# Kernel tuning notes

Measured on AMD Instinct MI355X. Metric: run time of the kernel, lower is better.

Reference implementation:

```python
import jax, jax.numpy as jnp
import numpy as np

CONTEXT_LENGTHS = [1, 3, 5, 7]
PADS = [(f - 1) // 2 for f in CONTEXT_LENGTHS]  # p(f) for odd f
B, H, L, DK = 2, 8, 1024, 64
C = H * DK  # conv channels = d_k * n_heads


def _conv1d(x, w, b, pad):
    # x: (b, C, L), w: (C, C, f), b: (C,) -- torch Conv1d semantics
    y = jax.lax.conv_general_dilated(
        x, w, window_strides=(1,), padding=[(pad, pad)],
        dimension_numbers=("NCH", "OIH", "NCH"))
    return y + b[None, :, None]


def _plane(a, w, b, pad, out_len):
    # Faithful to: conv(a.reshape(b, h*d_k, -1)).reshape(b, h, -1, d_k)[:, :, :out_len, :]
    bsz, h, l, d = a.shape
    y = _conv1d(a.reshape(bsz, h * d, l), w, b, pad)
    return y.reshape(bsz, h, -1, d)[:, :, :out_len, :]


def setup_inputs() -> dict:
    key = jax.random.key(0)
    ks = jax.random.split(key, 12)
    inp = {
        "Q": jax.random.normal(ks[0], (B, H, L, DK), jnp.float32),
        "K": jax.random.normal(ks[1], (B, H, L, DK), jnp.float32),
        "V": jax.random.normal(ks[2], (B, H, L, DK), jnp.float32),
        # causal mask: True = masked
        "attn_mask": jnp.broadcast_to(
            jnp.triu(jnp.ones((L, L), jnp.bool_), k=1), (B, H, L, L)),
    }
    for i, f in enumerate(CONTEXT_LENGTHS):
        scale = 1.0 / np.sqrt(C * f)
        inp[f"conv_w{i}"] = jax.random.normal(ks[3 + i], (C, C, f), jnp.float32) * scale
        inp[f"conv_b{i}"] = jax.random.normal(ks[7 + i], (C,), jnp.float32) * scale
    return inp


def reference(Q, K, V, attn_mask,
              conv_w0, conv_b0, conv_w1, conv_b1,
              conv_w2, conv_b2, conv_w3, conv_b3):
    ws = [conv_w0, conv_w1, conv_w2, conv_w3]
    bs = [conv_b0, conv_b1, conv_b2, conv_b3]
    b, h, l, d_k = Q.shape
    l_k = K.shape[2]
    p = len(CONTEXT_LENGTHS)
    Q_l = [_plane(Q, ws[i], bs[i], PADS[i], l) for i in range(p)]
    K_l = [_plane(K, ws[i], bs[i], PADS[i], l_k) for i in range(p)]
    # replicate torch.cat(dim=0).reshape(b, h, p, l, d) exactly (row-major)
    Q_p = jnp.concatenate(Q_l, axis=0).reshape(b, h, p, l, d_k)
    K_p = jnp.concatenate(K_l, axis=0).reshape(b, h, p, l_k, d_k)
    scores = jnp.einsum("bhpqd,bhpkd->bhpqk", Q_p, K_p) / np.sqrt(d_k).astype(np.float32)
    scores = jnp.where(attn_mask[:, :, None, :, :], jnp.float32(-1e9), scores)
    attn = jax.nn.softmax(scores, axis=-1)
    attn = jnp.max(attn, axis=2)  # max over planes -> (b,h,q,k)
    context = jnp.einsum("bhqk,bhkd->bhqd", attn, V)
    return (context, attn)
```

## Files before the change

### kernel.cpp

```cpp
#include <hip/hip_runtime.h>
#include <math.h>

#define C_CH 512
#define L_SEQ 1024
#define DK 64
#define NP 4
#define SC2 0.1803368801111f

typedef __attribute__((ext_vector_type(8))) short short8;
typedef __attribute__((ext_vector_type(4))) float f32x4;

__device__ __forceinline__ unsigned short f2bf(float f) {
    union { float f; unsigned u; } v; v.f = f;
    unsigned u = v.u;
    u += 0x7FFFu + ((u >> 16) & 1u);
    return (unsigned short)(u >> 16);
}

__device__ __forceinline__ void unpack_tri(int t, int& qt, int& kt) {
    int q = (int)((sqrtf(8.f * t + 1.f) - 1.f) * 0.5f);
    while ((q + 1) * (q + 2) / 2 <= t) q++;
    while (q * (q + 1) / 2 > t) q--;
    qt = q;
    kt = t - q * (q + 1) / 2;
}

__global__ __launch_bounds__(256)
void prep_w_kernel(const float* __restrict__ w0, const float* __restrict__ w1,
                   const float* __restrict__ w2, const float* __restrict__ w3,
                   unsigned short* __restrict__ Wb) {
    int tg = blockIdx.y;
    int plane, t;
    if (tg < 1)      { plane = 0; t = tg; }
    else if (tg < 4) { plane = 1; t = tg - 1; }
    else if (tg < 9) { plane = 2; t = tg - 4; }
    else             { plane = 3; t = tg - 9; }
    const float* W = (plane == 0) ? w0 : (plane == 1) ? w1 : (plane == 2) ? w2 : w3;
    const int f = (plane == 0) ? 1 : (plane == 1) ? 3 : (plane == 2) ? 5 : 7;

    int co = blockIdx.x * 32 + (threadIdx.x >> 3);
    int c8 = threadIdx.x & 7;
    for (int it = 0; it < 8; it++) {
        int ci = c8 * 8 + it * 64;
        unsigned short o[8];
#pragma unroll
        for (int j = 0; j < 8; j++)
            o[j] = f2bf(W[(size_t)(co * C_CH + ci + j) * f + t]);
        *(short8*)&Wb[((size_t)tg * C_CH + co) * C_CH + ci] = *(short8*)o;
    }
}

__global__ __launch_bounds__(256)
void prep_x_kernel(const float* __restrict__ Qin, const float* __restrict__ Kin,
                   unsigned short* __restrict__ Xt) {
    int tb = blockIdx.z;
    int tensor = tb >> 1, b = tb & 1;
    const float* X = (tensor ? Kin : Qin) + (size_t)b * C_CH * L_SEQ;
    unsigned short* O = Xt + (size_t)tb * 1032 * C_CH;

    int pos0 = blockIdx.x * 64;
    int ci0  = blockIdx.y * 64;
    int tid = threadIdx.x;

    __shared__ float tile[64][65];
    int tx = tid & 15, ty = tid >> 4;
#pragma unroll
    for (int rr = 0; rr < 4; rr++) {
        int ci_l = ty + rr * 16;
        float4 v = *(const float4*)&X[(size_t)(ci0 + ci_l) * L_SEQ + pos0 + tx * 4];
        tile[tx * 4 + 0][ci_l] = v.x;
        tile[tx * 4 + 1][ci_l] = v.y;
        tile[tx * 4 + 2][ci_l] = v.z;
        tile[tx * 4 + 3][ci_l] = v.w;
    }
    __syncthreads();
#pragma unroll
    for (int pp = 0; pp < 2; pp++) {
        int pos_l = (tid >> 3) + pp * 32;
        int cg = (tid & 7) * 8;
        unsigned short o[8];
#pragma unroll
        for (int j = 0; j < 8; j++) o[j] = f2bf(tile[pos_l][cg + j]);
        *(short8*)&O[(size_t)(pos0 + pos_l + 4) * C_CH + ci0 + cg] = *(short8*)o;
    }
    if (blockIdx.x == 0) {
        int r = tid >> 6, cc = tid & 63;
        O[(size_t)r * C_CH + ci0 + cc] = 0;
    }
    if (blockIdx.x == 15) {
        int r = tid >> 6, cc = tid & 63;
        O[(size_t)(1028 + r) * C_CH + ci0 + cc] = 0;
    }
}

__global__ __launch_bounds__(256)
void conv_mfma_kernel(const unsigned short* __restrict__ Xt,
                      const unsigned short* __restrict__ Wb,
                      const float* __restrict__ b0, const float* __restrict__ b1,
                      const float* __restrict__ b2, const float* __restrict__ b3,
                      unsigned short* __restrict__ Qp, unsigned short* __restrict__ Kp) {
    const int fs[4]   = {1, 3, 5, 7};
    const int toff[4] = {0, 1, 4, 9};
    int id = blockIdx.x;
    int plane, rel;
    if (id < 128)      { plane = 0; rel = id; }
    else if (id < 256) { plane = 1; rel = id - 128; }
    else if (id < 384) { plane = 3; rel = id - 256; }
    else               { plane = 2; rel = id - 384; }
    int co0  = (rel & 3) * 128;
    int pos0 = ((rel >> 2) & 7) * 128;
    int tb   = rel >> 5;
    int tensor = tb >> 1, b = tb & 1;
    const int f   = fs[plane];
    const int pad = (f - 1) >> 1;
    const int n   = f * 16;
    const float* bias = (plane == 0) ? b0 : (plane == 1) ? b1 : (plane == 2) ? b2 : b3;
    unsigned short* Out = tensor ? Kp : Qp;
    const unsigned short* Xbase = Xt + (size_t)tb * 1032 * C_CH;

    __shared__ __align__(16) unsigned short As[2][4096];
    __shared__ __align__(16) unsigned short Bs[2][4096];

    int tid  = threadIdx.x;
    int w    = tid >> 6;
    int lane = tid & 63;
    int l15  = lane & 15;
    int quad = lane >> 4;
    int wm = (w & 1) * 64;
    int wn = (w >> 1) * 64;
    int rowL = tid >> 2;
    int cS   = tid & 3;

    int woff[2];
#pragma unroll
    for (int rep = 0; rep < 2; rep++) {
        int r = rowL + rep * 64;
        int line = r >> 1;
        int sl = (((r & 1) << 2) | cS) ^ (line & 7);
        woff[rep] = line * 64 + sl * 8;
    }
    int aoff[4], boff[4];
#pragma unroll
    for (int mi = 0; mi < 4; mi++) {
        int r = wm + mi * 16 + l15;
        int line = r >> 1;
        aoff[mi] = line * 64 + ((((r & 1) << 2) | quad) ^ (line & 7)) * 8;
        int r2 = wn + mi * 16 + l15;
        int line2 = r2 >> 1;
        boff[mi] = line2 * 64 + ((((r2 & 1) << 2) | quad) ^ (line2 & 7)) * 8;
    }

    f32x4 acc[4][4];
#pragma unroll
    for (int mi = 0; mi < 4; mi++)
#pragma unroll
        for (int ni = 0; ni < 4; ni++) acc[mi][ni] = (f32x4){0.f, 0.f, 0.f, 0.f};

    short8 pA[2], pB[2];
    {
        const unsigned short* Wsl = Wb + ((size_t)toff[plane] * C_CH + co0) * C_CH;
        const unsigned short* Xsl = Xbase + (size_t)(pos0 - pad + 4) * C_CH;
#pragma unroll
        for (int rep = 0; rep < 2; rep++) {
            int r = rowL + rep * 64;
            pA[rep] = *(const short8*)&Wsl[(size_t)r * C_CH + cS * 8];
            pB[rep] = *(const short8*)&Xsl[(size_t)r * C_CH + cS * 8];
        }
    }

    for (int it = 0; it < n; it++) {
        int cur = it & 1;
        *(short8*)&As[cur][woff[0]] = pA[0];
        *(short8*)&As[cur][woff[1]] = pA[1];
        *(short8*)&Bs[cur][woff[0]] = pB[0];
        *(short8*)&Bs[cur][woff[1]] = pB[1];
        __syncthreads();

        if (it + 1 < n) {
            int t = (it + 1) >> 4, cc = (it + 1) & 15;
            const unsigned short* Wsl =
                Wb + ((size_t)(toff[plane] + t) * C_CH + co0) * C_CH + cc * 32;
            const unsigned short* Xsl =
                Xbase + (size_t)(pos0 + t - pad + 4) * C_CH + cc * 32;
#pragma unroll
            for (int rep = 0; rep < 2; rep++) {
                int r = rowL + rep * 64;
                pA[rep] = *(const short8*)&Wsl[(size_t)r * C_CH + cS * 8];
                pB[rep] = *(const short8*)&Xsl[(size_t)r * C_CH + cS * 8];
            }
        }

        short8 af[4], bf[4];
#pragma unroll
        for (int mi = 0; mi < 4; mi++) af[mi] = *(const short8*)&As[cur][aoff[mi]];
#pragma unroll
        for (int ni = 0; ni < 4; ni++) bf[ni] = *(const short8*)&Bs[cur][boff[ni]];
#pragma unroll
        for (int mi = 0; mi < 4; mi++)
#pragma unroll
            for (int ni = 0; ni < 4; ni++)
                acc[mi][ni] = __builtin_amdgcn_mfma_f32_16x16x32_bf16(
                    af[mi], bf[ni], acc[mi][ni], 0, 0, 0);
    }

#pragma unroll
    for (int mi = 0; mi < 4; mi++)
#pragma unroll
        for (int r = 0; r < 4; r++) {
            int co = co0 + wm + mi * 16 + quad * 4 + r;
            int h = co >> 6, cl = co & 63;
            float bv = bias[co];
            size_t sbase = (size_t)((b * 8 + h) * NP + plane) * L_SEQ * DK;
#pragma unroll
            for (int ni = 0; ni < 4; ni++) {
                int pos = pos0 + wn + ni * 16 + l15;
                int l = cl * 16 + (pos >> 6);
                int d = pos & 63;
                Out[sbase + (size_t)l * DK + d] = f2bf(acc[mi][ni][r] + bv);
            }
        }
}

__global__ __launch_bounds__(256)
void attn_stats_kernel(const unsigned short* __restrict__ Qb,
                       const unsigned short* __restrict__ Kb,
                       float* __restrict__ lsum) {
    int qt, kt;
    unpack_tri(blockIdx.x, qt, kt);
    int bh = blockIdx.y;
    int tid = threadIdx.x;
    int q0 = qt * 64, k0 = kt * 64;
    bool diag = (kt == qt);

    int b2 = bh >> 3, h2 = bh & 7;
    int plane  = b2 * 2 + (h2 >> 2);
    int b_orig = (h2 >> 1) & 1;
    int h_base = (h2 & 1) * 4;
    int w = tid >> 6, lane = tid & 63, l15 = lane & 15, quad = lane >> 4;

    float l[NP][4];
#pragma unroll
    for (int p = 0; p < NP; p++)
        for (int r = 0; r < 4; r++) l[p][r] = 0.f;

#pragma unroll
    for (int p = 0; p < NP; p++) {
        size_t slice = (size_t)((b_orig * 8 + h_base + p) * NP + plane);
        const unsigned short* kb = Kb + slice * L_SEQ * DK;
        const unsigned short* qrow =
            Qb + (slice * L_SEQ + (size_t)(q0 + w * 16 + l15)) * DK + quad * 8;
        short8 qa0 = *(const short8*)(qrow);
        short8 qa1 = *(const short8*)(qrow + 32);

        f32x4 c[4];
#pragma unroll
        for (int s = 0; s < 4; s++) {
            const unsigned short* kr = kb + (size_t)(k0 + s * 16 + l15) * DK + quad * 8;
            short8 kb0 = *(const short8*)(kr);
            short8 kb1 = *(const short8*)(kr + 32);
            f32x4 acc = {0.f, 0.f, 0.f, 0.f};
            acc = __builtin_amdgcn_mfma_f32_16x16x32_bf16(qa0, kb0, acc, 0, 0, 0);
            acc = __builtin_amdgcn_mfma_f32_16x16x32_bf16(qa1, kb1, acc, 0, 0, 0);
            c[s] = acc;
        }
#pragma unroll
        for (int r = 0; r < 4; r++) {
            int row_local = quad * 4 + r + w * 16;
#pragma unroll
            for (int s = 0; s < 4; s++) {
                float x = c[s][r] * SC2;
                if (diag && (s * 16 + l15 > row_local)) x = -1e30f;
                l[p][r] += exp2f(x);
            }
        }
    }

    size_t base = (size_t)(bh * 16 + qt) * (NP * 64);
#pragma unroll
    for (int p = 0; p < NP; p++)
#pragma unroll
        for (int r = 0; r < 4; r++) {
            float ll = l[p][r];
            ll += __shfl_xor(ll, 1);
            ll += __shfl_xor(ll, 2);
            ll += __shfl_xor(ll, 4);
            ll += __shfl_xor(ll, 8);
            if (l15 == 0)
                unsafeAtomicAdd(&lsum[base + p * 64 + (w * 16 + quad * 4 + r)], ll);
        }
}

__global__ __launch_bounds__(256)
void attn_combine_kernel(const float* __restrict__ lsum,
                         float* __restrict__ fstats,
                         float* __restrict__ out_ctx, float* __restrict__ out_attn) {
    int qt = blockIdx.x, bh = blockIdx.y;
    int tid = threadIdx.x;
    size_t sb = (size_t)(bh * 16 + qt) * (NP * 64);
    fstats[sb + tid] = __log2f(lsum[sb + tid]);

    int r = tid >> 2, c = (tid & 3) * 16;
    float4 z = make_float4(0.f, 0.f, 0.f, 0.f);
    size_t cbase = ((size_t)bh * L_SEQ + qt * 64 + r) * DK + c;
#pragma unroll
    for (int j = 0; j < 4; j++)
        *(float4*)&out_ctx[cbase + j * 4] = z;

    int kz = (qt + 1) * 64;
    size_t abase = ((size_t)bh * L_SEQ + qt * 64 + r) * L_SEQ;
    for (int k = kz + (tid & 3) * 4; k < L_SEQ; k += 16)
        *(float4*)&out_attn[abase + k] = z;
}

__global__ __launch_bounds__(256)
void attn_apply_kernel(const unsigned short* __restrict__ Qb,
                       const unsigned short* __restrict__ Kb,
                       const float* __restrict__ V,
                       const float* __restrict__ fstats,
                       float* __restrict__ out_ctx, float* __restrict__ out_attn) {
    int qt, kt;
    unpack_tri(blockIdx.x, qt, kt);
    int bh = blockIdx.y;
    int tid = threadIdx.x;
    int q0 = qt * 64, k0 = kt * 64;
    bool diag = (kt == qt);

    int b2 = bh >> 3, h2 = bh & 7;
    int plane  = b2 * 2 + (h2 >> 2);
    int b_orig = (h2 >> 1) & 1;
    int h_base = (h2 & 1) * 4;
    int w = tid >> 6, lane = tid & 63, l15 = lane & 15, quad = lane >> 4;

    __shared__ float zsm[NP * 64];
    __shared__ __align__(16) unsigned short ast[64 * 80];
    __shared__ __align__(16) unsigned short vts[64 * 80];

    zsm[tid] = fstats[(size_t)(bh * 16 + qt) * (NP * 64) + tid];

    const unsigned short* kbase[NP];
    short8 qa[NP][2];
#pragma unroll
    for (int p = 0; p < NP; p++) {
        size_t slice = (size_t)((b_orig * 8 + h_base + p) * NP + plane);
        kbase[p] = Kb + slice * L_SEQ * DK;
        const unsigned short* qrow =
            Qb + (slice * L_SEQ + (size_t)(q0 + w * 16 + l15)) * DK + quad * 8;
        qa[p][0] = *(const short8*)(qrow);
        qa[p][1] = *(const short8*)(qrow + 32);
    }

    {
        int kl = tid >> 2, db = (tid & 3) * 16;
        const float* vr = V + ((size_t)bh * L_SEQ + k0 + kl) * DK + db;
        float vv[16];
        *(float4*)&vv[0]  = *(const float4*)(vr);
        *(float4*)&vv[4]  = *(const float4*)(vr + 4);
        *(float4*)&vv[8]  = *(const float4*)(vr + 8);
        *(float4*)&vv[12] = *(const float4*)(vr + 12);
#pragma unroll
        for (int j = 0; j < 16; j++)
            vts[(db + j) * 80 + kl] = f2bf(vv[j]);
    }
    __syncthreads();

    float run[4][4];
#pragma unroll
    for (int s = 0; s < 4; s++)
        for (int r = 0; r < 4; r++) run[s][r] = -1e30f;

#pragma unroll
    for (int p = 0; p < NP; p++) {
        f32x4 c[4];
#pragma unroll
        for (int s = 0; s < 4; s++) {
            const unsigned short* kr =
                kbase[p] + (size_t)(k0 + s * 16 + l15) * DK + quad * 8;
            short8 kb0 = *(const short8*)(kr);
            short8 kb1 = *(const short8*)(kr + 32);
            f32x4 acc = {0.f, 0.f, 0.f, 0.f};
            acc = __builtin_amdgcn_mfma_f32_16x16x32_bf16(qa[p][0], kb0, acc, 0, 0, 0);
            acc = __builtin_amdgcn_mfma_f32_16x16x32_bf16(qa[p][1], kb1, acc, 0, 0, 0);
            c[s] = acc;
        }
#pragma unroll
        for (int r = 0; r < 4; r++) {
            float zp = zsm[p * 64 + (quad * 4 + r + w * 16)];
#pragma unroll
            for (int s = 0; s < 4; s++)
                run[s][r] = fmaxf(run[s][r], c[s][r] * SC2 - zp);
        }
    }

#pragma unroll
    for (int s = 0; s < 4; s++)
#pragma unroll
        for (int r = 0; r < 4; r++) {
            int qloc = w * 16 + quad * 4 + r;
            bool masked = diag && (s * 16 + l15 > qloc);
            float a = masked ? 0.f : exp2f(run[s][r]);
            out_attn[((size_t)bh * L_SEQ + q0 + qloc) * L_SEQ + k0 + s * 16 + l15] = a;
            ast[qloc * 80 + s * 16 + l15] = f2bf(a);
        }

    f32x4 ctxc[4];
#pragma unroll
    for (int ds = 0; ds < 4; ds++) ctxc[ds] = (f32x4){0.f, 0.f, 0.f, 0.f};
    short8 af0 = *(const short8*)&ast[(w * 16 + l15) * 80 + quad * 8];
    short8 af1 = *(const short8*)&ast[(w * 16 + l15) * 80 + 32 + quad * 8];
#pragma unroll
    for (int ds = 0; ds < 4; ds++) {
        short8 bf0 = *(const short8*)&vts[(ds * 16 + l15) * 80 + quad * 8];
        short8 bf1 = *(const short8*)&vts[(ds * 16 + l15) * 80 + 32 + quad * 8];
        ctxc[ds] = __builtin_amdgcn_mfma_f32_16x16x32_bf16(af0, bf0, ctxc[ds], 0, 0, 0);
        ctxc[ds] = __builtin_amdgcn_mfma_f32_16x16x32_bf16(af1, bf1, ctxc[ds], 0, 0, 0);
    }

#pragma unroll
    for (int ds = 0; ds < 4; ds++)
#pragma unroll
        for (int r = 0; r < 4; r++) {
            int qg = q0 + w * 16 + quad * 4 + r;
            unsafeAtomicAdd(&out_ctx[((size_t)bh * L_SEQ + qg) * DK + ds * 16 + l15],
                            ctxc[ds][r]);
        }
}

extern "C" void kernel_launch(void* const* d_in, const int* in_sizes, int n_in,
                              void* d_out, int out_size, void* d_ws, size_t ws_size,
                              hipStream_t stream) {
    const float* Q  = (const float*)d_in[0];
    const float* K  = (const float*)d_in[1];
    const float* V  = (const float*)d_in[2];
    const float* w0 = (const float*)d_in[4];
    const float* b0 = (const float*)d_in[5];
    const float* w1 = (const float*)d_in[6];
    const float* b1 = (const float*)d_in[7];
    const float* w2 = (const float*)d_in[8];
    const float* b2 = (const float*)d_in[9];
    const float* w3 = (const float*)d_in[10];
    const float* b3 = (const float*)d_in[11];

    char* ws = (char*)d_ws;
    unsigned short* Wb = (unsigned short*)(ws);
    unsigned short* Xt = (unsigned short*)(ws + 8388608);
    unsigned short* Qp = (unsigned short*)(ws + 12615680);
    unsigned short* Kp = (unsigned short*)(ws + 21004288);
    float* lsum   = (float*)(ws + 8388608);
    float* fstats = (float*)(ws + 8388608 + 262144);

    float* out_ctx  = (float*)d_out;
    float* out_attn = out_ctx + 1048576;

    prep_w_kernel<<<dim3(16, 16), 256, 0, stream>>>(w0, w1, w2, w3, Wb);
    prep_x_kernel<<<dim3(16, 8, 4), 256, 0, stream>>>(Q, K, Xt);
    conv_mfma_kernel<<<dim3(512), 256, 0, stream>>>(Xt, Wb, b0, b1, b2, b3, Qp, Kp);
    hipMemsetAsync(lsum, 0, 262144, stream);
    attn_stats_kernel<<<dim3(136, 16), 256, 0, stream>>>(Qp, Kp, lsum);
    attn_combine_kernel<<<dim3(16, 16), 256, 0, stream>>>(lsum, fstats, out_ctx, out_attn);
    attn_apply_kernel<<<dim3(136, 16), 256, 0, stream>>>(Qp, Kp, V, fstats,
                                                         out_ctx, out_attn);
}
```

Measured before the change: 355.0 us.

## Group key tiles per block and replace atomics with partial-sum reduction

The stats and apply kernels now give each block a contiguous run of up to four key tiles for one query tile, instead of one (q,k) tile pair per block. This cuts the grid from 136 to 40 blocks per head and reuses the loaded Q fragments across tiles. Atomic adds for the row sums and context are replaced by per-group partial buffers, which the combine kernel and a new ctx_reduce kernel sum, so the memset goes away. The trade-off is fewer blocks, which lowers parallelism, plus an extra launch and more workspace traffic. The apply loop uses double-buffered V smem with a single barrier per iteration.

```diff
diff --git a/kernel.cpp b/kernel.cpp
--- a/kernel.cpp
+++ b/kernel.cpp
@@ -17,12 +17,20 @@
     return (unsigned short)(u >> 16);
 }
 
-__device__ __forceinline__ void unpack_tri(int t, int& qt, int& kt) {
-    int q = (int)((sqrtf(8.f * t + 1.f) - 1.f) * 0.5f);
-    while ((q + 1) * (q + 2) / 2 <= t) q++;
-    while (q * (q + 1) / 2 > t) q--;
+__device__ __forceinline__ void unpack_group(int G, int& qt, int& kt0, int& kt1,
+                                             int& j, int& ng) {
+    int q = 15, cum = 0, jj = 0;
+    for (; q >= 0; q--) {
+        int g = (q + 4) >> 2;
+        if (G < cum + g) { jj = G - cum; break; }
+        cum += g;
+    }
     qt = q;
-    kt = t - q * (q + 1) / 2;
+    ng = (q + 4) >> 2;
+    j = jj;
+    int n = q + 1;
+    kt0 = (jj * n) / ng;
+    kt1 = ((jj + 1) * n) / ng;
 }
 
 __global__ __launch_bounds__(256)
@@ -44,8 +52,8 @@
         int ci = c8 * 8 + it * 64;
         unsigned short o[8];
 #pragma unroll
-        for (int j = 0; j < 8; j++)
-            o[j] = f2bf(W[(size_t)(co * C_CH + ci + j) * f + t]);
+        for (int jj = 0; jj < 8; jj++)
+            o[jj] = f2bf(W[(size_t)(co * C_CH + ci + jj) * f + t]);
         *(short8*)&Wb[((size_t)tg * C_CH + co) * C_CH + ci] = *(short8*)o;
     }
 }
@@ -80,7 +88,7 @@
         int cg = (tid & 7) * 8;
         unsigned short o[8];
 #pragma unroll
-        for (int j = 0; j < 8; j++) o[j] = f2bf(tile[pos_l][cg + j]);
+        for (int jj = 0; jj < 8; jj++) o[jj] = f2bf(tile[pos_l][cg + jj]);
         *(short8*)&O[(size_t)(pos0 + pos_l + 4) * C_CH + ci0 + cg] = *(short8*)o;
     }
     if (blockIdx.x == 0) {
@@ -224,13 +232,12 @@
 __global__ __launch_bounds__(256)
 void attn_stats_kernel(const unsigned short* __restrict__ Qb,
                        const unsigned short* __restrict__ Kb,
-                       float* __restrict__ lsum) {
-    int qt, kt;
-    unpack_tri(blockIdx.x, qt, kt);
+                       float* __restrict__ pl) {
+    int qt, kt0, kt1, j, ng;
+    unpack_group(blockIdx.x, qt, kt0, kt1, j, ng);
     int bh = blockIdx.y;
     int tid = threadIdx.x;
-    int q0 = qt * 64, k0 = kt * 64;
-    bool diag = (kt == qt);
+    int q0 = qt * 64;
 
     int b2 = bh >> 3, h2 = bh & 7;
     int plane  = b2 * 2 + (h2 >> 2);
@@ -238,44 +245,54 @@
     int h_base = (h2 & 1) * 4;
     int w = tid >> 6, lane = tid & 63, l15 = lane & 15, quad = lane >> 4;
 
+    const unsigned short* kbase[NP];
+    short8 qa[NP][2];
+#pragma unroll
+    for (int p = 0; p < NP; p++) {
+        size_t slice = (size_t)((b_orig * 8 + h_base + p) * NP + plane);
+        kbase[p] = Kb + slice * L_SEQ * DK;
+        const unsigned short* qrow =
+            Qb + (slice * L_SEQ + (size_t)(q0 + w * 16 + l15)) * DK + quad * 8;
+        qa[p][0] = *(const short8*)(qrow);
+        qa[p][1] = *(const short8*)(qrow + 32);
+    }
+
     float l[NP][4];
 #pragma unroll
     for (int p = 0; p < NP; p++)
         for (int r = 0; r < 4; r++) l[p][r] = 0.f;
 
-#pragma unroll
-    for (int p = 0; p < NP; p++) {
-        size_t slice = (size_t)((b_orig * 8 + h_base + p) * NP + plane);
-        const unsigned short* kb = Kb + slice * L_SEQ * DK;
-        const unsigned short* qrow =
-            Qb + (slice * L_SEQ + (size_t)(q0 + w * 16 + l15)) * DK + quad * 8;
-        short8 qa0 = *(const short8*)(qrow);
-        short8 qa1 = *(const short8*)(qrow + 32);
-
-        f32x4 c[4];
-#pragma unroll
-        for (int s = 0; s < 4; s++) {
-            const unsigned short* kr = kb + (size_t)(k0 + s * 16 + l15) * DK + quad * 8;
-            short8 kb0 = *(const short8*)(kr);
-            short8 kb1 = *(const short8*)(kr + 32);
-            f32x4 acc = {0.f, 0.f, 0.f, 0.f};
-            acc = __builtin_amdgcn_mfma_f32_16x16x32_bf16(qa0, kb0, acc, 0, 0, 0);
-            acc = __builtin_amdgcn_mfma_f32_16x16x32_bf16(qa1, kb1, acc, 0, 0, 0);
-            c[s] = acc;
-        }
-#pragma unroll
-        for (int r = 0; r < 4; r++) {
-            int row_local = quad * 4 + r + w * 16;
+    for (int kt = kt0; kt < kt1; kt++) {
+        int k0 = kt * 64;
+        bool diag = (kt == qt);
+#pragma unroll
+        for (int p = 0; p < NP; p++) {
+            f32x4 c[4];
 #pragma unroll
             for (int s = 0; s < 4; s++) {
-                float x = c[s][r] * SC2;
-                if (diag && (s * 16 + l15 > row_local)) x = -1e30f;
-                l[p][r] += exp2f(x);
-            }
-        }
-    }
-
-    size_t base = (size_t)(bh * 16 + qt) * (NP * 64);
+                const unsigned short* kr =
+                    kbase[p] + (size_t)(k0 + s * 16 + l15) * DK + quad * 8;
+                short8 kb0 = *(const short8*)(kr);
+                short8 kb1 = *(const short8*)(kr + 32);
+                f32x4 acc = {0.f, 0.f, 0.f, 0.f};
+                acc = __builtin_amdgcn_mfma_f32_16x16x32_bf16(qa[p][0], kb0, acc, 0, 0, 0);
+                acc = __builtin_amdgcn_mfma_f32_16x16x32_bf16(qa[p][1], kb1, acc, 0, 0, 0);
+                c[s] = acc;
+            }
+#pragma unroll
+            for (int r = 0; r < 4; r++) {
+                int row_local = quad * 4 + r + w * 16;
+#pragma unroll
+                for (int s = 0; s < 4; s++) {
+                    float x = c[s][r] * SC2;
+                    if (diag && (s * 16 + l15 > row_local)) x = -1e30f;
+                    l[p][r] += exp2f(x);
+                }
+            }
+        }
+    }
+
+    size_t base = ((size_t)(bh * 16 + qt) * 4 + j) * 256;
 #pragma unroll
     for (int p = 0; p < NP; p++)
 #pragma unroll
@@ -286,26 +303,26 @@
             ll += __shfl_xor(ll, 4);
             ll += __shfl_xor(ll, 8);
             if (l15 == 0)
-                unsafeAtomicAdd(&lsum[base + p * 64 + (w * 16 + quad * 4 + r)], ll);
-        }
-}
-
-__global__ __launch_bounds__(256)
-void attn_combine_kernel(const float* __restrict__ lsum,
+                pl[base + p * 64 + (w * 16 + quad * 4 + r)] = ll;
+        }
+}
+
+__global__ __launch_bounds__(256)
+void attn_combine_kernel(const float* __restrict__ pl,
                          float* __restrict__ fstats,
-                         float* __restrict__ out_ctx, float* __restrict__ out_attn) {
+                         float* __restrict__ out_attn) {
     int qt = blockIdx.x, bh = blockIdx.y;
     int tid = threadIdx.x;
-    size_t sb = (size_t)(bh * 16 + qt) * (NP * 64);
-    fstats[sb + tid] = __log2f(lsum[sb + tid]);
-
-    int r = tid >> 2, c = (tid & 3) * 16;
+    int ng = (qt + 4) >> 2;
+    size_t sb = (size_t)(bh * 16 + qt) * 4 * 256;
+
+    float l = 0.f;
+    for (int g = 0; g < ng; g++)
+        l += pl[sb + (size_t)g * 256 + tid];
+    fstats[(size_t)(bh * 16 + qt) * 256 + tid] = __log2f(l);
+
+    int r = tid >> 2;
     float4 z = make_float4(0.f, 0.f, 0.f, 0.f);
-    size_t cbase = ((size_t)bh * L_SEQ + qt * 64 + r) * DK + c;
-#pragma unroll
-    for (int j = 0; j < 4; j++)
-        *(float4*)&out_ctx[cbase + j * 4] = z;
-
     int kz = (qt + 1) * 64;
     size_t abase = ((size_t)bh * L_SEQ + qt * 64 + r) * L_SEQ;
     for (int k = kz + (tid & 3) * 4; k < L_SEQ; k += 16)
@@ -317,13 +334,12 @@
                        const unsigned short* __restrict__ Kb,
                        const float* __restrict__ V,
                        const float* __restrict__ fstats,
-                       float* __restrict__ out_ctx, float* __restrict__ out_attn) {
-    int qt, kt;
-    unpack_tri(blockIdx.x, qt, kt);
+                       float* __restrict__ pctx, float* __restrict__ out_attn) {
+    int qt, kt0, kt1, j, ng;
+    unpack_group(blockIdx.x, qt, kt0, kt1, j, ng);
     int bh = blockIdx.y;
     int tid = threadIdx.x;
-    int q0 = qt * 64, k0 = kt * 64;
-    bool diag = (kt == qt);
+    int q0 = qt * 64;
 
     int b2 = bh >> 3, h2 = bh & 7;
     int plane  = b2 * 2 + (h2 >> 2);
@@ -333,9 +349,9 @@
 
     __shared__ float zsm[NP * 64];
     __shared__ __align__(16) unsigned short ast[64 * 80];
-    __shared__ __align__(16) unsigned short vts[64 * 80];
-
-    zsm[tid] = fstats[(size_t)(bh * 16 + qt) * (NP * 64) + tid];
+    __shared__ __align__(16) unsigned short vts[2][64 * 80];
+
+    zsm[tid] = fstats[(size_t)(bh * 16 + qt) * 256 + tid];
 
     const unsigned short* kbase[NP];
     short8 qa[NP][2];
@@ -349,80 +365,118 @@
         qa[p][1] = *(const short8*)(qrow + 32);
     }
 
-    {
-        int kl = tid >> 2, db = (tid & 3) * 16;
-        const float* vr = V + ((size_t)bh * L_SEQ + k0 + kl) * DK + db;
-        float vv[16];
-        *(float4*)&vv[0]  = *(const float4*)(vr);
-        *(float4*)&vv[4]  = *(const float4*)(vr + 4);
-        *(float4*)&vv[8]  = *(const float4*)(vr + 8);
-        *(float4*)&vv[12] = *(const float4*)(vr + 12);
-#pragma unroll
-        for (int j = 0; j < 16; j++)
-            vts[(db + j) * 80 + kl] = f2bf(vv[j]);
-    }
-    __syncthreads();
-
-    float run[4][4];
-#pragma unroll
-    for (int s = 0; s < 4; s++)
-        for (int r = 0; r < 4; r++) run[s][r] = -1e30f;
-
-#pragma unroll
-    for (int p = 0; p < NP; p++) {
-        f32x4 c[4];
-#pragma unroll
-        for (int s = 0; s < 4; s++) {
-            const unsigned short* kr =
-                kbase[p] + (size_t)(k0 + s * 16 + l15) * DK + quad * 8;
-            short8 kb0 = *(const short8*)(kr);
-            short8 kb1 = *(const short8*)(kr + 32);
-            f32x4 acc = {0.f, 0.f, 0.f, 0.f};
-            acc = __builtin_amdgcn_mfma_f32_16x16x32_bf16(qa[p][0], kb0, acc, 0, 0, 0);
-            acc = __builtin_amdgcn_mfma_f32_16x16x32_bf16(qa[p][1], kb1, acc, 0, 0, 0);
-            c[s] = acc;
-        }
-#pragma unroll
-        for (int r = 0; r < 4; r++) {
-            float zp = zsm[p * 64 + (quad * 4 + r + w * 16)];
-#pragma unroll
-            for (int s = 0; s < 4; s++)
-                run[s][r] = fmaxf(run[s][r], c[s][r] * SC2 - zp);
-        }
-    }
-
-#pragma unroll
-    for (int s = 0; s < 4; s++)
+    f32x4 ctxc[4];
+#pragma unroll
+    for (int ds = 0; ds < 4; ds++) ctxc[ds] = (f32x4){0.f, 0.f, 0.f, 0.f};
+
+    for (int kt = kt0; kt < kt1; kt++) {
+        int k0 = kt * 64;
+        bool diag = (kt == qt);
+        unsigned short* vb = vts[kt & 1];
+
+        {
+            int kl = tid >> 2, db = (tid & 3) * 16;
+            const float* vr = V + ((size_t)bh * L_SEQ + k0 + kl) * DK + db;
+            float vv[16];
+            *(float4*)&vv[0]  = *(const float4*)(vr);
+            *(float4*)&vv[4]  = *(const float4*)(vr + 4);
+            *(float4*)&vv[8]  = *(const float4*)(vr + 8);
+            *(float4*)&vv[12] = *(const float4*)(vr + 12);
+#pragma unroll
+            for (int jj = 0; jj < 16; jj++)
+                vb[(db + jj) * 80 + kl] = f2bf(vv[jj]);
+        }
+        __syncthreads();
+
+        float run[4][4];
+#pragma unroll
+        for (int s = 0; s < 4; s++)
+            for (int r = 0; r < 4; r++) run[s][r] = -1e30f;
+
+#pragma unroll
+        for (int p = 0; p < NP; p++) {
+            f32x4 c[4];
+#pragma unroll
+            for (int s = 0; s < 4; s++) {
+                const unsigned short* kr =
+                    kbase[p] + (size_t)(k0 + s * 16 + l15) * DK + quad * 8;
+                short8 kb0 = *(const short8*)(kr);
+                short8 kb1 = *(const short8*)(kr + 32);
+                f32x4 acc = {0.f, 0.f, 0.f, 0.f};
+                acc = __builtin_amdgcn_mfma_f32_16x16x32_bf16(qa[p][0], kb0, acc, 0, 0, 0);
+                acc = __builtin_amdgcn_mfma_f32_16x16x32_bf16(qa[p][1], kb1, acc, 0, 0, 0);
+                c[s] = acc;
+            }
+#pragma unroll
+            for (int r = 0; r < 4; r++) {
+                float zp = zsm[p * 64 + (quad * 4 + r + w * 16)];
+#pragma unroll
+                for (int s = 0; s < 4; s++)
+                    run[s][r] = fmaxf(run[s][r], c[s][r] * SC2 - zp);
+            }
+        }
+
+#pragma unroll
+        for (int s = 0; s < 4; s++)
+#pragma unroll
+            for (int r = 0; r < 4; r++) {
+                int qloc = w * 16 + quad * 4 + r;
+                bool masked = diag && (s * 16 + l15 > qloc);
+                float a = masked ? 0.f : exp2f(run[s][r]);
+                out_attn[((size_t)bh * L_SEQ + q0 + qloc) * L_SEQ + k0 + s * 16 + l15] = a;
+                ast[qloc * 80 + s * 16 + l15] = f2bf(a);
+            }
+
+        short8 af0 = *(const short8*)&ast[(w * 16 + l15) * 80 + quad * 8];
+        short8 af1 = *(const short8*)&ast[(w * 16 + l15) * 80 + 32 + quad * 8];
+#pragma unroll
+        for (int ds = 0; ds < 4; ds++) {
+            short8 bf0 = *(const short8*)&vb[(ds * 16 + l15) * 80 + quad * 8];
+            short8 bf1 = *(const short8*)&vb[(ds * 16 + l15) * 80 + 32 + quad * 8];
+            ctxc[ds] = __builtin_amdgcn_mfma_f32_16x16x32_bf16(af0, bf0, ctxc[ds], 0, 0, 0);
+            ctxc[ds] = __builtin_amdgcn_mfma_f32_16x16x32_bf16(af1, bf1, ctxc[ds], 0, 0, 0);
+        }
+    }
+
+    size_t pbase = ((size_t)(bh * 16 + qt) * 4 + j) * 4096;
+#pragma unroll
+    for (int ds = 0; ds < 4; ds++)
 #pragma unroll
         for (int r = 0; r < 4; r++) {
             int qloc = w * 16 + quad * 4 + r;
-            bool masked = diag && (s * 16 + l15 > qloc);
-            float a = masked ? 0.f : exp2f(run[s][r]);
-            out_attn[((size_t)bh * L_SEQ + q0 + qloc) * L_SEQ + k0 + s * 16 + l15] = a;
-            ast[qloc * 80 + s * 16 + l15] = f2bf(a);
-        }
-
-    f32x4 ctxc[4];
-#pragma unroll
-    for (int ds = 0; ds < 4; ds++) ctxc[ds] = (f32x4){0.f, 0.f, 0.f, 0.f};
-    short8 af0 = *(const short8*)&ast[(w * 16 + l15) * 80 + quad * 8];
-    short8 af1 = *(const short8*)&ast[(w * 16 + l15) * 80 + 32 + quad * 8];
-#pragma unroll
-    for (int ds = 0; ds < 4; ds++) {
-        short8 bf0 = *(const short8*)&vts[(ds * 16 + l15) * 80 + quad * 8];
-        short8 bf1 = *(const short8*)&vts[(ds * 16 + l15) * 80 + 32 + quad * 8];
-        ctxc[ds] = __builtin_amdgcn_mfma_f32_16x16x32_bf16(af0, bf0, ctxc[ds], 0, 0, 0);
-        ctxc[ds] = __builtin_amdgcn_mfma_f32_16x16x32_bf16(af1, bf1, ctxc[ds], 0, 0, 0);
-    }
-
-#pragma unroll
-    for (int ds = 0; ds < 4; ds++)
-#pragma unroll
-        for (int r = 0; r < 4; r++) {
-            int qg = q0 + w * 16 + quad * 4 + r;
-            unsafeAtomicAdd(&out_ctx[((size_t)bh * L_SEQ + qg) * DK + ds * 16 + l15],
-                            ctxc[ds][r]);
-        }
+            pctx[pbase + (size_t)qloc * 64 + ds * 16 + l15] = ctxc[ds][r];
+        }
+}
+
+__global__ __launch_bounds__(256)
+void ctx_reduce_kernel(const float* __restrict__ pctx, float* __restrict__ out_ctx) {
+    int qt = blockIdx.x, bh = blockIdx.y;
+    int tid = threadIdx.x;
+    int ng = (qt + 4) >> 2;
+    size_t base = (size_t)(bh * 16 + qt) * 4 * 4096;
+    int row = tid >> 2, c = (tid & 3) * 16;
+    size_t off = (size_t)row * 64 + c;
+
+    float4 a0 = *(const float4*)&pctx[base + off];
+    float4 a1 = *(const float4*)&pctx[base + off + 4];
+    float4 a2 = *(const float4*)&pctx[base + off + 8];
+    float4 a3 = *(const float4*)&pctx[base + off + 12];
+    for (int g = 1; g < ng; g++) {
+        size_t gb = base + (size_t)g * 4096 + off;
+        float4 b0 = *(const float4*)&pctx[gb];
+        float4 b1 = *(const float4*)&pctx[gb + 4];
+        float4 b2 = *(const float4*)&pctx[gb + 8];
+        float4 b3 = *(const float4*)&pctx[gb + 12];
+        a0.x += b0.x; a0.y += b0.y; a0.z += b0.z; a0.w += b0.w;
+        a1.x += b1.x; a1.y += b1.y; a1.z += b1.z; a1.w += b1.w;
+        a2.x += b2.x; a2.y += b2.y; a2.z += b2.z; a2.w += b2.w;
+        a3.x += b3.x; a3.y += b3.y; a3.z += b3.z; a3.w += b3.w;
+    }
+    size_t ob = ((size_t)bh * L_SEQ + qt * 64 + row) * DK + c;
+    *(float4*)&out_ctx[ob]      = a0;
+    *(float4*)&out_ctx[ob + 4]  = a1;
+    *(float4*)&out_ctx[ob + 8]  = a2;
+    *(float4*)&out_ctx[ob + 12] = a3;
 }
 
 extern "C" void kernel_launch(void* const* d_in, const int* in_sizes, int n_in,
@@ -445,8 +499,9 @@
     unsigned short* Xt = (unsigned short*)(ws + 8388608);
     unsigned short* Qp = (unsigned short*)(ws + 12615680);
     unsigned short* Kp = (unsigned short*)(ws + 21004288);
-    float* lsum   = (float*)(ws + 8388608);
-    float* fstats = (float*)(ws + 8388608 + 262144);
+    float* pctx        = (float*)(ws + 29392896);
+    float* pl     = (float*)(ws + 8388608);
+    float* fstats = (float*)(ws + 8388608 + 1048576);
 
     float* out_ctx  = (float*)d_out;
     float* out_attn = out_ctx + 1048576;
@@ -454,9 +509,9 @@
     prep_w_kernel<<<dim3(16, 16), 256, 0, stream>>>(w0, w1, w2, w3, Wb);
     prep_x_kernel<<<dim3(16, 8, 4), 256, 0, stream>>>(Q, K, Xt);
     conv_mfma_kernel<<<dim3(512), 256, 0, stream>>>(Xt, Wb, b0, b1, b2, b3, Qp, Kp);
-    hipMemsetAsync(lsum, 0, 262144, stream);
-    attn_stats_kernel<<<dim3(136, 16), 256, 0, stream>>>(Qp, Kp, lsum);
-    attn_combine_kernel<<<dim3(16, 16), 256, 0, stream>>>(lsum, fstats, out_ctx, out_attn);
-    attn_apply_kernel<<<dim3(136, 16), 256, 0, stream>>>(Qp, Kp, V, fstats,
-                                                         out_ctx, out_attn);
-}
+    attn_stats_kernel<<<dim3(40, 16), 256, 0, stream>>>(Qp, Kp, pl);
+    attn_combine_kernel<<<dim3(16, 16), 256, 0, stream>>>(pl, fstats, out_attn);
+    attn_apply_kernel<<<dim3(40, 16), 256, 0, stream>>>(Qp, Kp, V, fstats,
+                                                        pctx, out_attn);
+    ctx_reduce_kernel<<<dim3(16, 16), 256, 0, stream>>>(pctx, out_ctx);
+}
```

Measured after the change: 355.4 us. About the same (+0.1%).

## Split context GEMM into separate kernel and replace atomics with per-tile partial sums

Applied to the files above, without the earlier changes.

Attention stats now write per-(q-tile, k-tile) partial row sums to a buffer that the combine kernel reduces, which removes the memset and float atomics. Stats and apply kernels move to 128-row query tiles with 512 threads, and warps whose rows are fully masked skip early. The P·V product is taken out of the apply kernel and done in a new ctx_gemm kernel that rereads the fp32 attention output and V, so the output-side atomics go away. The cost is an extra kernel launch plus a reread of the attention matrix from global memory.

```diff
diff --git a/kernel.cpp b/kernel.cpp
--- a/kernel.cpp
+++ b/kernel.cpp
@@ -17,12 +17,14 @@
     return (unsigned short)(u >> 16);
 }
 
-__device__ __forceinline__ void unpack_tri(int t, int& qt, int& kt) {
-    int q = (int)((sqrtf(8.f * t + 1.f) - 1.f) * 0.5f);
-    while ((q + 1) * (q + 2) / 2 <= t) q++;
-    while (q * (q + 1) / 2 > t) q--;
-    qt = q;
-    kt = t - q * (q + 1) / 2;
+__device__ __forceinline__ void unpack_tile128(int G, int& qt8, int& kt) {
+    int cum = 0;
+    for (int q8 = 7; q8 >= 0; q8--) {
+        int c = 2 * q8 + 2;
+        if (G < cum + c) { qt8 = q8; kt = G - cum; return; }
+        cum += c;
+    }
+    qt8 = 0; kt = 0;
 }
 
 __global__ __launch_bounds__(256)
@@ -44,8 +46,8 @@
         int ci = c8 * 8 + it * 64;
         unsigned short o[8];
 #pragma unroll
-        for (int j = 0; j < 8; j++)
-            o[j] = f2bf(W[(size_t)(co * C_CH + ci + j) * f + t]);
+        for (int jj = 0; jj < 8; jj++)
+            o[jj] = f2bf(W[(size_t)(co * C_CH + ci + jj) * f + t]);
         *(short8*)&Wb[((size_t)tg * C_CH + co) * C_CH + ci] = *(short8*)o;
     }
 }
@@ -80,7 +82,7 @@
         int cg = (tid & 7) * 8;
         unsigned short o[8];
 #pragma unroll
-        for (int j = 0; j < 8; j++) o[j] = f2bf(tile[pos_l][cg + j]);
+        for (int jj = 0; jj < 8; jj++) o[jj] = f2bf(tile[pos_l][cg + jj]);
         *(short8*)&O[(size_t)(pos0 + pos_l + 4) * C_CH + ci0 + cg] = *(short8*)o;
     }
     if (blockIdx.x == 0) {
@@ -221,22 +223,24 @@
         }
 }
 
-__global__ __launch_bounds__(256)
+__global__ __launch_bounds__(512)
 void attn_stats_kernel(const unsigned short* __restrict__ Qb,
                        const unsigned short* __restrict__ Kb,
-                       float* __restrict__ lsum) {
-    int qt, kt;
-    unpack_tri(blockIdx.x, qt, kt);
+                       float* __restrict__ pl) {
+    int qt8, kt;
+    unpack_tile128(blockIdx.x, qt8, kt);
     int bh = blockIdx.y;
     int tid = threadIdx.x;
-    int q0 = qt * 64, k0 = kt * 64;
-    bool diag = (kt == qt);
+    int w = tid >> 6, lane = tid & 63, l15 = lane & 15, quad = lane >> 4;
+    int q0 = qt8 * 128, k0 = kt * 64;
+    int qrow0 = q0 + w * 16;
+
+    if (qrow0 + 15 < k0) return;
 
     int b2 = bh >> 3, h2 = bh & 7;
     int plane  = b2 * 2 + (h2 >> 2);
     int b_orig = (h2 >> 1) & 1;
     int h_base = (h2 & 1) * 4;
-    int w = tid >> 6, lane = tid & 63, l15 = lane & 15, quad = lane >> 4;
 
     float l[NP][4];
 #pragma unroll
@@ -248,7 +252,7 @@
         size_t slice = (size_t)((b_orig * 8 + h_base + p) * NP + plane);
         const unsigned short* kb = Kb + slice * L_SEQ * DK;
         const unsigned short* qrow =
-            Qb + (slice * L_SEQ + (size_t)(q0 + w * 16 + l15)) * DK + quad * 8;
+            Qb + (slice * L_SEQ + (size_t)(qrow0 + l15)) * DK + quad * 8;
         short8 qa0 = *(const short8*)(qrow);
         short8 qa1 = *(const short8*)(qrow + 32);
 
@@ -265,17 +269,18 @@
         }
 #pragma unroll
         for (int r = 0; r < 4; r++) {
-            int row_local = quad * 4 + r + w * 16;
+            int qg = qrow0 + quad * 4 + r;
 #pragma unroll
             for (int s = 0; s < 4; s++) {
                 float x = c[s][r] * SC2;
-                if (diag && (s * 16 + l15 > row_local)) x = -1e30f;
+                if (k0 + s * 16 + l15 > qg) x = -1e30f;
                 l[p][r] += exp2f(x);
             }
         }
     }
 
-    size_t base = (size_t)(bh * 16 + qt) * (NP * 64);
+    int qt64 = qt8 * 2 + (w >> 2);
+    size_t base = ((size_t)(bh * 16 + qt64) * 16 + kt) * 256;
 #pragma unroll
     for (int p = 0; p < NP; p++)
 #pragma unroll
@@ -286,105 +291,96 @@
             ll += __shfl_xor(ll, 4);
             ll += __shfl_xor(ll, 8);
             if (l15 == 0)
-                unsafeAtomicAdd(&lsum[base + p * 64 + (w * 16 + quad * 4 + r)], ll);
+                pl[base + p * 64 + ((w & 3) * 16 + quad * 4 + r)] = ll;
         }
 }
 
 __global__ __launch_bounds__(256)
-void attn_combine_kernel(const float* __restrict__ lsum,
+void attn_combine_kernel(const float* __restrict__ pl,
                          float* __restrict__ fstats,
-                         float* __restrict__ out_ctx, float* __restrict__ out_attn) {
+                         float* __restrict__ out_attn) {
     int qt = blockIdx.x, bh = blockIdx.y;
     int tid = threadIdx.x;
-    size_t sb = (size_t)(bh * 16 + qt) * (NP * 64);
-    fstats[sb + tid] = __log2f(lsum[sb + tid]);
-
-    int r = tid >> 2, c = (tid & 3) * 16;
+    size_t sb = (size_t)(bh * 16 + qt) * 16 * 256;
+
+    float l = 0.f;
+    for (int kt = 0; kt <= qt; kt++)
+        l += pl[sb + (size_t)kt * 256 + tid];
+    fstats[(size_t)(bh * 16 + qt) * 256 + tid] = __log2f(l);
+
+    int r = tid >> 2;
     float4 z = make_float4(0.f, 0.f, 0.f, 0.f);
-    size_t cbase = ((size_t)bh * L_SEQ + qt * 64 + r) * DK + c;
-#pragma unroll
-    for (int j = 0; j < 4; j++)
-        *(float4*)&out_ctx[cbase + j * 4] = z;
-
     int kz = (qt + 1) * 64;
     size_t abase = ((size_t)bh * L_SEQ + qt * 64 + r) * L_SEQ;
     for (int k = kz + (tid & 3) * 4; k < L_SEQ; k += 16)
         *(float4*)&out_attn[abase + k] = z;
 }
 
-__global__ __launch_bounds__(256)
+__global__ __launch_bounds__(512)
 void attn_apply_kernel(const unsigned short* __restrict__ Qb,
                        const unsigned short* __restrict__ Kb,
-                       const float* __restrict__ V,
                        const float* __restrict__ fstats,
-                       float* __restrict__ out_ctx, float* __restrict__ out_attn) {
-    int qt, kt;
-    unpack_tri(blockIdx.x, qt, kt);
+                       float* __restrict__ out_attn) {
+    int qt8, kt;
+    unpack_tile128(blockIdx.x, qt8, kt);
     int bh = blockIdx.y;
     int tid = threadIdx.x;
-    int q0 = qt * 64, k0 = kt * 64;
-    bool diag = (kt == qt);
+    int w = tid >> 6, lane = tid & 63, l15 = lane & 15, quad = lane >> 4;
+    int q0 = qt8 * 128, k0 = kt * 64;
+    int qrow0 = q0 + w * 16;
+
+    __shared__ float zsm[512];
+    {
+        int p = tid >> 7, row = tid & 127;
+        int qt64 = qt8 * 2 + (row >> 6);
+        zsm[tid] = fstats[(size_t)(bh * 16 + qt64) * 256 + p * 64 + (row & 63)];
+    }
+    __syncthreads();
+
+    if (qrow0 + 15 < k0) {
+#pragma unroll
+        for (int s = 0; s < 4; s++)
+#pragma unroll
+            for (int r = 0; r < 4; r++) {
+                int qg = qrow0 + quad * 4 + r;
+                out_attn[((size_t)bh * L_SEQ + qg) * L_SEQ + k0 + s * 16 + l15] = 0.f;
+            }
+        return;
+    }
 
     int b2 = bh >> 3, h2 = bh & 7;
     int plane  = b2 * 2 + (h2 >> 2);
     int b_orig = (h2 >> 1) & 1;
     int h_base = (h2 & 1) * 4;
-    int w = tid >> 6, lane = tid & 63, l15 = lane & 15, quad = lane >> 4;
-
-    __shared__ float zsm[NP * 64];
-    __shared__ __align__(16) unsigned short ast[64 * 80];
-    __shared__ __align__(16) unsigned short vts[64 * 80];
-
-    zsm[tid] = fstats[(size_t)(bh * 16 + qt) * (NP * 64) + tid];
-
-    const unsigned short* kbase[NP];
-    short8 qa[NP][2];
+
+    float run[4][4];
+#pragma unroll
+    for (int s = 0; s < 4; s++)
+        for (int r = 0; r < 4; r++) run[s][r] = -1e30f;
+
 #pragma unroll
     for (int p = 0; p < NP; p++) {
         size_t slice = (size_t)((b_orig * 8 + h_base + p) * NP + plane);
-        kbase[p] = Kb + slice * L_SEQ * DK;
+        const unsigned short* kb = Kb + slice * L_SEQ * DK;
         const unsigned short* qrow =
-            Qb + (slice * L_SEQ + (size_t)(q0 + w * 16 + l15)) * DK + quad * 8;
-        qa[p][0] = *(const short8*)(qrow);
-        qa[p][1] = *(const short8*)(qrow + 32);
-    }
-
-    {
-        int kl = tid >> 2, db = (tid & 3) * 16;
-        const float* vr = V + ((size_t)bh * L_SEQ + k0 + kl) * DK + db;
-        float vv[16];
-        *(float4*)&vv[0]  = *(const float4*)(vr);
-        *(float4*)&vv[4]  = *(const float4*)(vr + 4);
-        *(float4*)&vv[8]  = *(const float4*)(vr + 8);
-        *(float4*)&vv[12] = *(const float4*)(vr + 12);
-#pragma unroll
-        for (int j = 0; j < 16; j++)
-            vts[(db + j) * 80 + kl] = f2bf(vv[j]);
-    }
-    __syncthreads();
-
-    float run[4][4];
-#pragma unroll
-    for (int s = 0; s < 4; s++)
-        for (int r = 0; r < 4; r++) run[s][r] = -1e30f;
-
-#pragma unroll
-    for (int p = 0; p < NP; p++) {
+            Qb + (slice * L_SEQ + (size_t)(qrow0 + l15)) * DK + quad * 8;
+        short8 qa0 = *(const short8*)(qrow);
+        short8 qa1 = *(const short8*)(qrow + 32);
+
         f32x4 c[4];
 #pragma unroll
         for (int s = 0; s < 4; s++) {
-            const unsigned short* kr =
-                kbase[p] + (size_t)(k0 + s * 16 + l15) * DK + quad * 8;
+            const unsigned short* kr = kb + (size_t)(k0 + s * 16 + l15) * DK + quad * 8;
             short8 kb0 = *(const short8*)(kr);
             short8 kb1 = *(const short8*)(kr + 32);
             f32x4 acc = {0.f, 0.f, 0.f, 0.f};
-            acc = __builtin_amdgcn_mfma_f32_16x16x32_bf16(qa[p][0], kb0, acc, 0, 0, 0);
-            acc = __builtin_amdgcn_mfma_f32_16x16x32_bf16(qa[p][1], kb1, acc, 0, 0, 0);
+            acc = __builtin_amdgcn_mfma_f32_16x16x32_bf16(qa0, kb0, acc, 0, 0, 0);
+            acc = __builtin_amdgcn_mfma_f32_16x16x32_bf16(qa1, kb1, acc, 0, 0, 0);
             c[s] = acc;
         }
 #pragma unroll
         for (int r = 0; r < 4; r++) {
-            float zp = zsm[p * 64 + (quad * 4 + r + w * 16)];
+            float zp = zsm[p * 128 + (w * 16 + quad * 4 + r)];
 #pragma unroll
             for (int s = 0; s < 4; s++)
                 run[s][r] = fmaxf(run[s][r], c[s][r] * SC2 - zp);
@@ -395,33 +391,77 @@
     for (int s = 0; s < 4; s++)
 #pragma unroll
         for (int r = 0; r < 4; r++) {
-            int qloc = w * 16 + quad * 4 + r;
-            bool masked = diag && (s * 16 + l15 > qloc);
-            float a = masked ? 0.f : exp2f(run[s][r]);
-            out_attn[((size_t)bh * L_SEQ + q0 + qloc) * L_SEQ + k0 + s * 16 + l15] = a;
-            ast[qloc * 80 + s * 16 + l15] = f2bf(a);
-        }
-
-    f32x4 ctxc[4];
-#pragma unroll
-    for (int ds = 0; ds < 4; ds++) ctxc[ds] = (f32x4){0.f, 0.f, 0.f, 0.f};
-    short8 af0 = *(const short8*)&ast[(w * 16 + l15) * 80 + quad * 8];
-    short8 af1 = *(const short8*)&ast[(w * 16 + l15) * 80 + 32 + quad * 8];
-#pragma unroll
-    for (int ds = 0; ds < 4; ds++) {
-        short8 bf0 = *(const short8*)&vts[(ds * 16 + l15) * 80 + quad * 8];
-        short8 bf1 = *(const short8*)&vts[(ds * 16 + l15) * 80 + 32 + quad * 8];
-        ctxc[ds] = __builtin_amdgcn_mfma_f32_16x16x32_bf16(af0, bf0, ctxc[ds], 0, 0, 0);
-        ctxc[ds] = __builtin_amdgcn_mfma_f32_16x16x32_bf16(af1, bf1, ctxc[ds], 0, 0, 0);
-    }
-
-#pragma unroll
-    for (int ds = 0; ds < 4; ds++)
+            int qg = qrow0 + quad * 4 + r;
+            int kg = k0 + s * 16 + l15;
+            float a = (kg > qg) ? 0.f : exp2f(run[s][r]);
+            out_attn[((size_t)bh * L_SEQ + qg) * L_SEQ + kg] = a;
+        }
+}
+
+__global__ __launch_bounds__(512)
+void ctx_gemm_kernel(const float* __restrict__ attn, const float* __restrict__ V,
+                     float* __restrict__ out_ctx) {
+    int qt = 15 - blockIdx.x;
+    int bh = blockIdx.y;
+    int tid = threadIdx.x;
+    int w = tid >> 6, lane = tid & 63, l15 = lane & 15, quad = lane >> 4;
+    int q0 = qt * 64;
+    int nk = (qt + 1) * 64;
+    int wq = (w & 3) * 16;
+    int ds0 = (w >> 2) * 2;
+
+    __shared__ __align__(16) unsigned short vts[64 * 136];
+
+    const float* Arow = attn + ((size_t)bh * L_SEQ + q0 + wq + l15) * L_SEQ;
+    const float* Vb = V + (size_t)bh * L_SEQ * DK;
+
+    f32x4 acc[2];
+    acc[0] = (f32x4){0.f, 0.f, 0.f, 0.f};
+    acc[1] = (f32x4){0.f, 0.f, 0.f, 0.f};
+
+    for (int c0 = 0; c0 < nk; c0 += 128) {
+        int rem = min(128, nk - c0);
+        __syncthreads();
+        {
+            int kl = tid >> 2, db = (tid & 3) * 16;
+            if (kl < rem) {
+                const float* vr = Vb + (size_t)(c0 + kl) * DK + db;
+                float vv[16];
+                *(float4*)&vv[0]  = *(const float4*)(vr);
+                *(float4*)&vv[4]  = *(const float4*)(vr + 4);
+                *(float4*)&vv[8]  = *(const float4*)(vr + 8);
+                *(float4*)&vv[12] = *(const float4*)(vr + 12);
+#pragma unroll
+                for (int jj = 0; jj < 16; jj++)
+                    vts[(db + jj) * 136 + kl] = f2bf(vv[jj]);
+            }
+        }
+        __syncthreads();
+
+        int nss = rem >> 5;
+        for (int ss = 0; ss < nss; ss++) {
+            int kk = c0 + ss * 32 + quad * 8;
+            float4 a0 = *(const float4*)&Arow[kk];
+            float4 a1 = *(const float4*)&Arow[kk + 4];
+            unsigned short af[8];
+            af[0] = f2bf(a0.x); af[1] = f2bf(a0.y); af[2] = f2bf(a0.z); af[3] = f2bf(a0.w);
+            af[4] = f2bf(a1.x); af[5] = f2bf(a1.y); af[6] = f2bf(a1.z); af[7] = f2bf(a1.w);
+            short8 afv = *(short8*)af;
+#pragma unroll
+            for (int t = 0; t < 2; t++) {
+                short8 bf = *(const short8*)&vts[((ds0 + t) * 16 + l15) * 136 +
+                                                 ss * 32 + quad * 8];
+                acc[t] = __builtin_amdgcn_mfma_f32_16x16x32_bf16(afv, bf, acc[t], 0, 0, 0);
+            }
+        }
+    }
+
+#pragma unroll
+    for (int t = 0; t < 2; t++)
 #pragma unroll
         for (int r = 0; r < 4; r++) {
-            int qg = q0 + w * 16 + quad * 4 + r;
-            unsafeAtomicAdd(&out_ctx[((size_t)bh * L_SEQ + qg) * DK + ds * 16 + l15],
-                            ctxc[ds][r]);
+            int qg = q0 + wq + quad * 4 + r;
+            out_ctx[((size_t)bh * L_SEQ + qg) * DK + (ds0 + t) * 16 + l15] = acc[t][r];
         }
 }
 
@@ -445,8 +485,8 @@
     unsigned short* Xt = (unsigned short*)(ws + 8388608);
     unsigned short* Qp = (unsigned short*)(ws + 12615680);
     unsigned short* Kp = (unsigned short*)(ws + 21004288);
-    float* lsum   = (float*)(ws + 8388608);
-    float* fstats = (float*)(ws + 8388608 + 262144);
+    float* pl     = (float*)(ws);
+    float* fstats = (float*)(ws + 4194304);
 
     float* out_ctx  = (float*)d_out;
     float* out_attn = out_ctx + 1048576;
@@ -454,9 +494,8 @@
     prep_w_kernel<<<dim3(16, 16), 256, 0, stream>>>(w0, w1, w2, w3, Wb);
     prep_x_kernel<<<dim3(16, 8, 4), 256, 0, stream>>>(Q, K, Xt);
     conv_mfma_kernel<<<dim3(512), 256, 0, stream>>>(Xt, Wb, b0, b1, b2, b3, Qp, Kp);
-    hipMemsetAsync(lsum, 0, 262144, stream);
-    attn_stats_kernel<<<dim3(136, 16), 256, 0, stream>>>(Qp, Kp, lsum);
-    attn_combine_kernel<<<dim3(16, 16), 256, 0, stream>>>(lsum, fstats, out_ctx, out_attn);
-    attn_apply_kernel<<<dim3(136, 16), 256, 0, stream>>>(Qp, Kp, V, fstats,
-                                                         out_ctx, out_attn);
-}
+    attn_stats_kernel<<<dim3(72, 16), 512, 0, stream>>>(Qp, Kp, pl);
+    attn_combine_kernel<<<dim3(16, 16), 256, 0, stream>>>(pl, fstats, out_attn);
+    attn_apply_kernel<<<dim3(72, 16), 512, 0, stream>>>(Qp, Kp, fstats, out_attn);
+    ctx_gemm_kernel<<<dim3(16, 16), 512, 0, stream>>>(out_attn, V, out_ctx);
+}
```

Result: slower. 374.0 us (+5.4%).
